# Kernel optimization log

Measured on AMD Instinct MI355X. Metric: run time of the kernel, lower is better.

Reference implementation:

```python
import jax, jax.numpy as jnp
import numpy as np

B, D, C = 8192, 128, 1000
EPS = 1e-6      # torch nn.PairwiseDistance default eps (added to the difference)
LAMBD = 0.1


def setup_inputs() -> dict:
    key = jax.random.key(0)
    k1, k2, k3 = jax.random.split(key, 3)
    return {
        "data": jax.random.normal(k1, (B, C), jnp.float32),
        "x": jax.random.normal(k2, (B, D), jnp.float32),
        "y": jax.random.randint(k3, (B,), 0, C),
    }


def _pdist_matrix(x):
    # torch PairwiseDistance(p=2): ||x_i - x_j + eps||_2, computed without
    # materializing the [B,B,D] difference tensor.
    sq = jnp.sum(x * x, axis=1)          # [B]
    s = jnp.sum(x, axis=1)               # [B]
    n = x.shape[1]
    g = x @ x.T                          # [B,B] Gram
    d2 = (sq[:, None] + sq[None, :] - 2.0 * g
          + 2.0 * EPS * (s[:, None] - s[None, :]) + n * EPS * EPS)
    return jnp.sqrt(jnp.maximum(d2, 0.0))


def reference(data, x, y):
    # cross-entropy (mean reduction, as nn.CrossEntropyLoss default)
    logp = jax.nn.log_softmax(data, axis=-1)
    loss_acc = -jnp.mean(jnp.take_along_axis(logp, y[:, None], axis=1))

    dist = _pdist_matrix(x)                       # [B,B]
    same = y[:, None] == y[None, :]               # label mask
    first_pos = jnp.argmax(same, axis=1)          # first index with same label (pos[0] in torch)
    d_pos = jnp.take_along_axis(dist, first_pos[:, None], axis=1)[:, 0]  # [B]
    d_tot = jnp.sum(dist, axis=1)                 # [B]
    loss_feature = jnp.sum(d_pos / (d_tot - d_pos))

    loss = loss_acc + LAMBD * loss_feature
    return (loss, loss_acc, loss_feature)
```

## Files before the change

### kernel.cpp

```cpp
#include <hip/hip_runtime.h>
#include <math.h>

#define B 8192
#define D 128
#define C 1000
#define EPS 1e-6f
#define LAMBD 0.1f

#define OFF_DTOT 2
#define OFF_E (2 + B)
#define OFF_F (2 + 2 * B)
#define OFF_DPOS (2 + 3 * B)
#define OFF_FO (2 + 4 * B)
#define OFF_XBF 33792

typedef __attribute__((ext_vector_type(8))) short short8;
typedef __attribute__((ext_vector_type(4))) float floatx4;

__device__ inline unsigned short f2bf(float f) {
    union { float f; unsigned u; } v; v.f = f;
    unsigned u = v.u;
    return (unsigned short)((u + 0x7fffu + ((u >> 16) & 1u)) >> 16);
}

__global__ void __launch_bounds__(256)
k_rowstats(const float* __restrict__ x, const int* __restrict__ y, float* ws) {
    int row = blockIdx.x * 4 + (threadIdx.x >> 6);
    int lane = threadIdx.x & 63;
    const float2* x2 = (const float2*)x;
    float2 v = x2[row * 64 + lane];
    float sq = v.x * v.x + v.y * v.y;
    float s = v.x + v.y;
    for (int o = 32; o; o >>= 1) {
        sq += __shfl_xor(sq, o);
        s += __shfl_xor(s, o);
    }
    ushort2 p = { f2bf(v.x), f2bf(v.y) };
    ushort2* xrow = (ushort2*)((unsigned short*)(ws + OFF_XBF) + row * 128);
    xrow[(((lane >> 2) ^ (row & 7)) << 2) + (lane & 3)] = p;
    if (lane == 0) {
        ws[OFF_E + row] = sq + 2.f * EPS * s;
        ws[OFF_F + row] = sq - 2.f * EPS * s;
        atomicMin((unsigned*)(ws + OFF_FO) + y[row], (unsigned)row);
    }
}

__global__ void __launch_bounds__(256)
k_ce(const float* __restrict__ data, const int* __restrict__ y, float* ws) {
    int row = blockIdx.x * 4 + (threadIdx.x >> 6);
    int lane = threadIdx.x & 63;
    const float* dr = data + (size_t)row * C;
    const float4* dr4 = (const float4*)dr;

    float4 v[4];
    float m = -1e30f;
#pragma unroll
    for (int k = 0; k < 4; k++) {
        int idx = k * 64 + lane;
        if (idx < C / 4) {
            v[k] = dr4[idx];
            m = fmaxf(fmaxf(fmaxf(m, v[k].x), fmaxf(v[k].y, v[k].z)), v[k].w);
        }
    }
    for (int o = 32; o; o >>= 1) m = fmaxf(m, __shfl_xor(m, o));

    float sum = 0.f;
#pragma unroll
    for (int k = 0; k < 4; k++) {
        int idx = k * 64 + lane;
        if (idx < C / 4) {
            sum += __expf(v[k].x - m) + __expf(v[k].y - m) +
                   __expf(v[k].z - m) + __expf(v[k].w - m);
        }
    }
    for (int o = 32; o; o >>= 1) sum += __shfl_xor(sum, o);

    __shared__ float sp[4];
    if (lane == 0) {
        float lse = m + __logf(sum);
        sp[threadIdx.x >> 6] = lse - dr[y[row]];
    }
    __syncthreads();
    if (threadIdx.x == 0)
        atomicAdd(ws + 0, sp[0] + sp[1] + sp[2] + sp[3]);
}

__global__ void k_dpos(const float* __restrict__ x, const int* __restrict__ y,
                       float* ws) {
    int row = blockIdx.x * 4 + (threadIdx.x >> 6);
    int lane = threadIdx.x & 63;
    const unsigned* fo = (const unsigned*)(ws + OFF_FO);
    int fp = (int)fo[y[row]];
    float d0 = x[row * D + lane] - x[fp * D + lane] + EPS;
    float d1 = x[row * D + 64 + lane] - x[fp * D + 64 + lane] + EPS;
    float sq = d0 * d0 + d1 * d1;
    for (int o = 32; o; o >>= 1) sq += __shfl_xor(sq, o);
    if (lane == 0) ws[OFF_DPOS + row] = sqrtf(sq);
}

__global__ void __launch_bounds__(256)
k_gram_dtot(float* ws) {
    int bj = blockIdx.x, bi = blockIdx.y;
    if (bj < bi) return;
    bool offdiag = (bj != bi);

    __shared__ alignas(16) short lA[128 * 128];
    __shared__ alignas(16) short lB[128 * 128];
    __shared__ float sdrow[128];
    __shared__ float sdcol[128];
    int t = threadIdx.x;
    int i0 = bi * 128, j0 = bj * 128;

    const short8* xb8 = (const short8*)(ws + OFF_XBF);
#pragma unroll
    for (int it = 0; it < 8; ++it) {
        int idx = it * 256 + t;
        ((short8*)lA)[idx] = xb8[i0 * 16 + idx];
        ((short8*)lB)[idx] = xb8[j0 * 16 + idx];
    }
    if (t < 128) { sdrow[t] = 0.f; sdcol[t] = 0.f; }
    __syncthreads();

    int lane = t & 63, wid = t >> 6;
    int wm = wid >> 1, wn = wid & 1;
    int lo = lane & 15, hi = lane >> 4;

    floatx4 acc[4][4];
#pragma unroll
    for (int mr = 0; mr < 4; ++mr)
#pragma unroll
        for (int nr = 0; nr < 4; ++nr) acc[mr][nr] = (floatx4){0.f, 0.f, 0.f, 0.f};

#pragma unroll
    for (int kt = 0; kt < 4; ++kt) {
        short8 af[4], bg[4];
        int ch = kt * 4 + hi;
#pragma unroll
        for (int mr = 0; mr < 4; ++mr) {
            int r = wm * 64 + mr * 16 + lo;
            af[mr] = *(const short8*)&lA[r * 128 + ((ch ^ (r & 7)) << 3)];
        }
#pragma unroll
        for (int nr = 0; nr < 4; ++nr) {
            int r = wn * 64 + nr * 16 + lo;
            bg[nr] = *(const short8*)&lB[r * 128 + ((ch ^ (r & 7)) << 3)];
        }
#pragma unroll
        for (int mr = 0; mr < 4; ++mr)
#pragma unroll
            for (int nr = 0; nr < 4; ++nr)
                acc[mr][nr] = __builtin_amdgcn_mfma_f32_16x16x32_bf16(
                    af[mr], bg[nr], acc[mr][nr], 0, 0, 0);
    }

    const float* e = ws + OFF_E;
    const float* f = ws + OFF_F;
    float* dtot = ws + OFF_DTOT;
    const float deps2 = (float)D * EPS * EPS;

    float er[4][4];
#pragma unroll
    for (int mr = 0; mr < 4; ++mr)
#pragma unroll
        for (int rg = 0; rg < 4; ++rg)
            er[mr][rg] = e[i0 + wm * 64 + mr * 16 + hi * 4 + rg] + deps2;
    float fc[4];
#pragma unroll
    for (int nr = 0; nr < 4; ++nr) fc[nr] = f[j0 + wn * 64 + nr * 16 + lo];

    float rs[4][4], cs[4];
#pragma unroll
    for (int mr = 0; mr < 4; ++mr)
#pragma unroll
        for (int rg = 0; rg < 4; ++rg) rs[mr][rg] = 0.f;
#pragma unroll
    for (int nr = 0; nr < 4; ++nr) cs[nr] = 0.f;

#pragma unroll
    for (int mr = 0; mr < 4; ++mr)
#pragma unroll
        for (int nr = 0; nr < 4; ++nr)
#pragma unroll
            for (int rg = 0; rg < 4; ++rg) {
                float d2 = er[mr][rg] + fc[nr] - 2.f * acc[mr][nr][rg];
                float d = sqrtf(fmaxf(d2, 0.f));
                rs[mr][rg] += d;
                cs[nr] += d;
            }

#pragma unroll
    for (int mr = 0; mr < 4; ++mr)
#pragma unroll
        for (int rg = 0; rg < 4; ++rg) {
            float v = rs[mr][rg];
            v += __shfl_xor(v, 1);
            v += __shfl_xor(v, 2);
            v += __shfl_xor(v, 4);
            v += __shfl_xor(v, 8);
            if (lo == 0) atomicAdd(&sdrow[wm * 64 + mr * 16 + hi * 4 + rg], v);
        }
    if (offdiag) {
#pragma unroll
        for (int nr = 0; nr < 4; ++nr) {
            float v = cs[nr];
            v += __shfl_xor(v, 16);
            v += __shfl_xor(v, 32);
            if (hi == 0) atomicAdd(&sdcol[wn * 64 + nr * 16 + lo], v);
        }
    }
    __syncthreads();
    if (t < 128) {
        atomicAdd(&dtot[i0 + t], sdrow[t]);
        if (offdiag) atomicAdd(&dtot[j0 + t], sdcol[t]);
    }
}

__global__ void __launch_bounds__(1024)
k_featout(const float* __restrict__ ws, float* __restrict__ out) {
    int t = threadIdx.x;
    const float* dtot = ws + OFF_DTOT;
    const float* dpos = ws + OFF_DPOS;
    float r = 0.f;
#pragma unroll
    for (int k = 0; k < B / 1024; k++) {
        int i = k * 1024 + t;
        float dp = dpos[i], dt = dtot[i];
        r += dp / (dt - dp);
    }
    for (int o = 32; o; o >>= 1) r += __shfl_xor(r, o);
    __shared__ float sm[16];
    if ((t & 63) == 0) sm[t >> 6] = r;
    __syncthreads();
    if (t == 0) {
        float lf = 0.f;
#pragma unroll
        for (int w = 0; w < 16; w++) lf += sm[w];
        float la = ws[0] / (float)B;
        out[0] = la + LAMBD * lf;
        out[1] = la;
        out[2] = lf;
    }
}

extern "C" void kernel_launch(void* const* d_in, const int* in_sizes, int n_in,
                              void* d_out, int out_size, void* d_ws, size_t ws_size,
                              hipStream_t stream) {
    const float* data = (const float*)d_in[0];
    const float* x = (const float*)d_in[1];
    const int* y = (const int*)d_in[2];
    float* out = (float*)d_out;
    float* ws = (float*)d_ws;

    (void)hipMemsetAsync(ws, 0, (2 + B) * sizeof(float), stream);
    (void)hipMemsetAsync(ws + OFF_FO, 0xFF, C * sizeof(unsigned), stream);
    k_rowstats<<<B / 4, 256, 0, stream>>>(x, y, ws);
    k_ce<<<B / 4, 256, 0, stream>>>(data, y, ws);
    k_dpos<<<B / 4, 256, 0, stream>>>(x, y, ws);
    k_gram_dtot<<<dim3(64, 64), 256, 0, stream>>>(ws);
    k_featout<<<1, 1024, 0, stream>>>(ws, out);
}
```

Measured before the change: 179.6 us.

## Rework Gram-dtot kernel into persistent balanced band pairs with register-resident A tiles

Replaces the 64x64 grid, where half the blocks exit immediately, with 512 blocks. Each block walks a balanced pair of row bands (p and 63-p) over upper-triangle tiles. The A band fragments are loaded once into registers and reused across tiles, and B fragments are read directly from global memory instead of being staged in LDS. Row sums are flushed with global atomics only when the band changes, and column sums go straight to global atomics. The sqrt is replaced by x*rsqrt with a clamp at deps2, and launch bounds request 2 blocks per CU. The cost is more global atomics, no LDS reuse of the B tile, and higher register pressure.

After: 152.5 us. -15.1%, faster.

```diff
diff --git a/kernel.cpp b/kernel.cpp
--- a/kernel.cpp
+++ b/kernel.cpp
@@ -98,121 +98,118 @@
     if (lane == 0) ws[OFF_DPOS + row] = sqrtf(sq);
 }
 
-__global__ void __launch_bounds__(256)
+__global__ void __launch_bounds__(256, 2)
 k_gram_dtot(float* ws) {
-    int bj = blockIdx.x, bi = blockIdx.y;
-    if (bj < bi) return;
-    bool offdiag = (bj != bi);
-
-    __shared__ alignas(16) short lA[128 * 128];
-    __shared__ alignas(16) short lB[128 * 128];
-    __shared__ float sdrow[128];
-    __shared__ float sdcol[128];
-    int t = threadIdx.x;
-    int i0 = bi * 128, j0 = bj * 128;
-
-    const short8* xb8 = (const short8*)(ws + OFF_XBF);
-#pragma unroll
-    for (int it = 0; it < 8; ++it) {
-        int idx = it * 256 + t;
-        ((short8*)lA)[idx] = xb8[i0 * 16 + idx];
-        ((short8*)lB)[idx] = xb8[j0 * 16 + idx];
-    }
-    if (t < 128) { sdrow[t] = 0.f; sdcol[t] = 0.f; }
-    __syncthreads();
-
-    int lane = t & 63, wid = t >> 6;
-    int wm = wid >> 1, wn = wid & 1;
-    int lo = lane & 15, hi = lane >> 4;
-
-    floatx4 acc[4][4];
-#pragma unroll
-    for (int mr = 0; mr < 4; ++mr)
-#pragma unroll
-        for (int nr = 0; nr < 4; ++nr) acc[mr][nr] = (floatx4){0.f, 0.f, 0.f, 0.f};
-
-#pragma unroll
-    for (int kt = 0; kt < 4; ++kt) {
-        short8 af[4], bg[4];
-        int ch = kt * 4 + hi;
-#pragma unroll
-        for (int mr = 0; mr < 4; ++mr) {
-            int r = wm * 64 + mr * 16 + lo;
-            af[mr] = *(const short8*)&lA[r * 128 + ((ch ^ (r & 7)) << 3)];
-        }
-#pragma unroll
-        for (int nr = 0; nr < 4; ++nr) {
-            int r = wn * 64 + nr * 16 + lo;
-            bg[nr] = *(const short8*)&lB[r * 128 + ((ch ^ (r & 7)) << 3)];
-        }
-#pragma unroll
-        for (int mr = 0; mr < 4; ++mr)
-#pragma unroll
-            for (int nr = 0; nr < 4; ++nr)
-                acc[mr][nr] = __builtin_amdgcn_mfma_f32_16x16x32_bf16(
-                    af[mr], bg[nr], acc[mr][nr], 0, 0, 0);
-    }
-
-    const float* e = ws + OFF_E;
-    const float* f = ws + OFF_F;
+    const int t = threadIdx.x;
+    const int lane = t & 63, wid = t >> 6;
+    const int wm = wid >> 1, wn = wid & 1;
+    const int lo = lane & 15, hi = lane >> 4;
+    const int p = blockIdx.x >> 4;
+    const int sub = blockIdx.x & 15;
+    const int b0 = p, b1 = 63 - p;
+    const int n0 = 64 - b0;
+
+    const short8* __restrict__ xb8 = (const short8*)(ws + OFF_XBF);
+    const float* __restrict__ e = ws + OFF_E;
+    const float* __restrict__ f = ws + OFF_F;
     float* dtot = ws + OFF_DTOT;
     const float deps2 = (float)D * EPS * EPS;
-
-    float er[4][4];
-#pragma unroll
-    for (int mr = 0; mr < 4; ++mr)
-#pragma unroll
-        for (int rg = 0; rg < 4; ++rg)
-            er[mr][rg] = e[i0 + wm * 64 + mr * 16 + hi * 4 + rg] + deps2;
-    float fc[4];
-#pragma unroll
-    for (int nr = 0; nr < 4; ++nr) fc[nr] = f[j0 + wn * 64 + nr * 16 + lo];
-
-    float rs[4][4], cs[4];
-#pragma unroll
-    for (int mr = 0; mr < 4; ++mr)
-#pragma unroll
-        for (int rg = 0; rg < 4; ++rg) rs[mr][rg] = 0.f;
-#pragma unroll
-    for (int nr = 0; nr < 4; ++nr) cs[nr] = 0.f;
-
-#pragma unroll
-    for (int mr = 0; mr < 4; ++mr)
-#pragma unroll
-        for (int nr = 0; nr < 4; ++nr)
-#pragma unroll
-            for (int rg = 0; rg < 4; ++rg) {
-                float d2 = er[mr][rg] + fc[nr] - 2.f * acc[mr][nr][rg];
-                float d = sqrtf(fmaxf(d2, 0.f));
-                rs[mr][rg] += d;
-                cs[nr] += d;
+    const int swz = lo & 7;
+
+    short8 af[4][4];
+    float er[4][4], rs[4][4];
+    int cur_band = -1;
+
+#define FLUSH_RS()                                                            \
+    {                                                                         \
+        _Pragma("unroll") for (int mr = 0; mr < 4; ++mr)                      \
+            _Pragma("unroll") for (int rg = 0; rg < 4; ++rg) {                \
+            float v = rs[mr][rg];                                             \
+            v += __shfl_xor(v, 1);                                            \
+            v += __shfl_xor(v, 2);                                            \
+            v += __shfl_xor(v, 4);                                            \
+            v += __shfl_xor(v, 8);                                            \
+            if (lo == 0)                                                      \
+                atomicAdd(&dtot[cur_band * 128 + wm * 64 + mr * 16 + hi * 4 + rg], v); \
+        }                                                                     \
+    }
+
+    for (int q = sub; q < 65; q += 16) {
+        int band = (q < n0) ? b0 : b1;
+        int j = (q < n0) ? b0 + q : b1 + (q - n0);
+
+        if (band != cur_band) {
+            if (cur_band >= 0) FLUSH_RS();
+            cur_band = band;
+#pragma unroll
+            for (int mr = 0; mr < 4; ++mr) {
+                int r = band * 128 + wm * 64 + mr * 16 + lo;
+#pragma unroll
+                for (int kt = 0; kt < 4; ++kt)
+                    af[kt][mr] = xb8[r * 16 + ((kt * 4 + hi) ^ swz)];
+#pragma unroll
+                for (int rg = 0; rg < 4; ++rg) {
+                    er[mr][rg] =
+                        e[band * 128 + wm * 64 + mr * 16 + hi * 4 + rg] + deps2;
+                    rs[mr][rg] = 0.f;
+                }
             }
-
-#pragma unroll
-    for (int mr = 0; mr < 4; ++mr)
-#pragma unroll
-        for (int rg = 0; rg < 4; ++rg) {
-            float v = rs[mr][rg];
-            v += __shfl_xor(v, 1);
-            v += __shfl_xor(v, 2);
-            v += __shfl_xor(v, 4);
-            v += __shfl_xor(v, 8);
-            if (lo == 0) atomicAdd(&sdrow[wm * 64 + mr * 16 + hi * 4 + rg], v);
-        }
-    if (offdiag) {
-#pragma unroll
-        for (int nr = 0; nr < 4; ++nr) {
-            float v = cs[nr];
-            v += __shfl_xor(v, 16);
-            v += __shfl_xor(v, 32);
-            if (hi == 0) atomicAdd(&sdcol[wn * 64 + nr * 16 + lo], v);
-        }
-    }
-    __syncthreads();
-    if (t < 128) {
-        atomicAdd(&dtot[i0 + t], sdrow[t]);
-        if (offdiag) atomicAdd(&dtot[j0 + t], sdcol[t]);
-    }
+        }
+
+        const int jr = j * 128 + wn * 64;
+        float fc[4];
+#pragma unroll
+        for (int nr = 0; nr < 4; ++nr) fc[nr] = f[jr + nr * 16 + lo];
+
+        floatx4 acc[4][4];
+#pragma unroll
+        for (int mr = 0; mr < 4; ++mr)
+#pragma unroll
+            for (int nr = 0; nr < 4; ++nr)
+                acc[mr][nr] = (floatx4){0.f, 0.f, 0.f, 0.f};
+
+#pragma unroll
+        for (int kt = 0; kt < 4; ++kt) {
+            short8 bg[4];
+#pragma unroll
+            for (int nr = 0; nr < 4; ++nr) {
+                int r = jr + nr * 16 + lo;
+                bg[nr] = xb8[r * 16 + ((kt * 4 + hi) ^ swz)];
+            }
+#pragma unroll
+            for (int mr = 0; mr < 4; ++mr)
+#pragma unroll
+                for (int nr = 0; nr < 4; ++nr)
+                    acc[mr][nr] = __builtin_amdgcn_mfma_f32_16x16x32_bf16(
+                        af[kt][mr], bg[nr], acc[mr][nr], 0, 0, 0);
+        }
+
+        float cs[4] = {0.f, 0.f, 0.f, 0.f};
+#pragma unroll
+        for (int mr = 0; mr < 4; ++mr)
+#pragma unroll
+            for (int nr = 0; nr < 4; ++nr)
+#pragma unroll
+                for (int rg = 0; rg < 4; ++rg) {
+                    float d2 = fmaf(-2.f, acc[mr][nr][rg], er[mr][rg]) + fc[nr];
+                    float pp = fmaxf(d2, deps2);
+                    float d = pp * __frsqrt_rn(pp);
+                    rs[mr][rg] += d;
+                    cs[nr] += d;
+                }
+
+        if (j != band) {
+#pragma unroll
+            for (int nr = 0; nr < 4; ++nr) {
+                float v = cs[nr];
+                v += __shfl_xor(v, 16);
+                v += __shfl_xor(v, 32);
+                if (hi == 0) atomicAdd(&dtot[jr + nr * 16 + lo], v);
+            }
+        }
+    }
+    if (cur_band >= 0) FLUSH_RS();
+#undef FLUSH_RS
 }
 
 __global__ void __launch_bounds__(1024)
@@ -256,6 +253,6 @@
     k_rowstats<<<B / 4, 256, 0, stream>>>(x, y, ws);
     k_ce<<<B / 4, 256, 0, stream>>>(data, y, ws);
     k_dpos<<<B / 4, 256, 0, stream>>>(x, y, ws);
-    k_gram_dtot<<<dim3(64, 64), 256, 0, stream>>>(ws);
+    k_gram_dtot<<<512, 256, 0, stream>>>(ws);
     k_featout<<<1, 1024, 0, stream>>>(ws, out);
 }
```

## Drop shared-memory dtot staging, fold zero-init into rowstats, use rsqrt sqrt

Applied to the files above, without the earlier changes.

The Gram kernel now adds row and column partial sums straight into the global dtot array with atomics, instead of staging them in shared arrays and using a trailing barrier. Zeroing dtot and the CE accumulator moves into k_rowstats, which removes one memset launch. The distance epilogue uses an fma, vector loads for e, and d = p*rsqrt(p) with a floor of deps2 in place of sqrtf. The trade-off is more global atomics per block and slightly different rounding in the distance values.

New measurement: 171.6 us. 1.05x faster.

```diff
diff --git a/kernel.cpp b/kernel.cpp
--- a/kernel.cpp
+++ b/kernel.cpp
@@ -7,11 +7,11 @@
 #define EPS 1e-6f
 #define LAMBD 0.1f
 
-#define OFF_DTOT 2
-#define OFF_E (2 + B)
-#define OFF_F (2 + 2 * B)
-#define OFF_DPOS (2 + 3 * B)
-#define OFF_FO (2 + 4 * B)
+#define OFF_DTOT 16
+#define OFF_E (16 + B)
+#define OFF_F (16 + 2 * B)
+#define OFF_DPOS (16 + 3 * B)
+#define OFF_FO (16 + 4 * B)
 #define OFF_XBF 33792
 
 typedef __attribute__((ext_vector_type(8))) short short8;
@@ -43,6 +43,8 @@
         ws[OFF_F + row] = sq - 2.f * EPS * s;
         atomicMin((unsigned*)(ws + OFF_FO) + y[row], (unsigned)row);
     }
+    if (lane == 1) ws[OFF_DTOT + row] = 0.f;
+    if (blockIdx.x == 0 && threadIdx.x == 0) ws[0] = 0.f;
 }
 
 __global__ void __launch_bounds__(256)
@@ -106,19 +108,16 @@
 
     __shared__ alignas(16) short lA[128 * 128];
     __shared__ alignas(16) short lB[128 * 128];
-    __shared__ float sdrow[128];
-    __shared__ float sdcol[128];
     int t = threadIdx.x;
     int i0 = bi * 128, j0 = bj * 128;
 
-    const short8* xb8 = (const short8*)(ws + OFF_XBF);
+    const short8* __restrict__ xb8 = (const short8*)(ws + OFF_XBF);
 #pragma unroll
     for (int it = 0; it < 8; ++it) {
         int idx = it * 256 + t;
         ((short8*)lA)[idx] = xb8[i0 * 16 + idx];
         ((short8*)lB)[idx] = xb8[j0 * 16 + idx];
     }
-    if (t < 128) { sdrow[t] = 0.f; sdcol[t] = 0.f; }
     __syncthreads();
 
     int lane = t & 63, wid = t >> 6;
@@ -158,23 +157,21 @@
     float* dtot = ws + OFF_DTOT;
     const float deps2 = (float)D * EPS * EPS;
 
-    float er[4][4];
-#pragma unroll
-    for (int mr = 0; mr < 4; ++mr)
-#pragma unroll
-        for (int rg = 0; rg < 4; ++rg)
-            er[mr][rg] = e[i0 + wm * 64 + mr * 16 + hi * 4 + rg] + deps2;
+    floatx4 er4[4];
+#pragma unroll
+    for (int mr = 0; mr < 4; ++mr)
+        er4[mr] = *(const floatx4*)&e[i0 + wm * 64 + mr * 16 + hi * 4];
     float fc[4];
 #pragma unroll
-    for (int nr = 0; nr < 4; ++nr) fc[nr] = f[j0 + wn * 64 + nr * 16 + lo];
-
-    float rs[4][4], cs[4];
+    for (int nr = 0; nr < 4; ++nr)
+        fc[nr] = f[j0 + wn * 64 + nr * 16 + lo] + deps2;
+
+    float rs[4][4];
+    float cs[4] = {0.f, 0.f, 0.f, 0.f};
 #pragma unroll
     for (int mr = 0; mr < 4; ++mr)
 #pragma unroll
         for (int rg = 0; rg < 4; ++rg) rs[mr][rg] = 0.f;
-#pragma unroll
-    for (int nr = 0; nr < 4; ++nr) cs[nr] = 0.f;
 
 #pragma unroll
     for (int mr = 0; mr < 4; ++mr)
@@ -182,8 +179,9 @@
         for (int nr = 0; nr < 4; ++nr)
 #pragma unroll
             for (int rg = 0; rg < 4; ++rg) {
-                float d2 = er[mr][rg] + fc[nr] - 2.f * acc[mr][nr][rg];
-                float d = sqrtf(fmaxf(d2, 0.f));
+                float d2 = fmaf(-2.f, acc[mr][nr][rg], er4[mr][rg] + fc[nr]);
+                float pp = fmaxf(d2, deps2);
+                float d = pp * __frsqrt_rn(pp);
                 rs[mr][rg] += d;
                 cs[nr] += d;
             }
@@ -197,7 +195,8 @@
             v += __shfl_xor(v, 2);
             v += __shfl_xor(v, 4);
             v += __shfl_xor(v, 8);
-            if (lo == 0) atomicAdd(&sdrow[wm * 64 + mr * 16 + hi * 4 + rg], v);
+            if (lo == 0)
+                atomicAdd(&dtot[i0 + wm * 64 + mr * 16 + hi * 4 + rg], v);
         }
     if (offdiag) {
 #pragma unroll
@@ -205,13 +204,8 @@
             float v = cs[nr];
             v += __shfl_xor(v, 16);
             v += __shfl_xor(v, 32);
-            if (hi == 0) atomicAdd(&sdcol[wn * 64 + nr * 16 + lo], v);
-        }
-    }
-    __syncthreads();
-    if (t < 128) {
-        atomicAdd(&dtot[i0 + t], sdrow[t]);
-        if (offdiag) atomicAdd(&dtot[j0 + t], sdcol[t]);
+            if (hi == 0) atomicAdd(&dtot[j0 + wn * 64 + nr * 16 + lo], v);
+        }
     }
 }
 
@@ -251,7 +245,6 @@
     float* out = (float*)d_out;
     float* ws = (float*)d_ws;
 
-    (void)hipMemsetAsync(ws, 0, (2 + B) * sizeof(float), stream);
     (void)hipMemsetAsync(ws + OFF_FO, 0xFF, C * sizeof(unsigned), stream);
     k_rowstats<<<B / 4, 256, 0, stream>>>(x, y, ws);
     k_ce<<<B / 4, 256, 0, stream>>>(data, y, ws);
```
